# Optimization experiments

Measured on AMD Instinct MI355X. Metric: run time of the kernel, lower is better.

## Reference

```python
import math
import jax, jax.numpy as jnp
import numpy as np

B, LD, LE = 8, 512, 512
D, H, DK, F, L, V = 1024, 16, 64, 4096, 3, 32000
EPS = 1e-5
NEG = -1000000000.0


def setup_inputs() -> dict:
    key = jax.random.key(0)
    ks = jax.random.split(key, 16)
    s = 0.02
    dec_inputs = jax.random.randint(ks[0], (B, LD), 0, V)
    # causal mask: True = masked out (matches masked_fill semantics)
    self_mask = jnp.broadcast_to(jnp.triu(jnp.ones((LD, LD), bool), k=1), (B, LD, LD))
    enc_output = jax.random.normal(ks[1], (B, LE, D), jnp.float32)
    encoder_mask = jnp.zeros((B, LD, LE), bool)  # no encoder padding
    embed = jax.random.normal(ks[2], (V, D), jnp.float32) * s
    # sinusoidal positional encoding, pe[:LD]
    pos = jnp.arange(LD, dtype=jnp.float32)[:, None]
    div = jnp.exp(jnp.arange(0, D, 2, dtype=jnp.float32) * (-math.log(10000.0) / D))
    pe = jnp.zeros((LD, D), jnp.float32)
    pe = pe.at[:, 0::2].set(jnp.sin(pos * div)).at[:, 1::2].set(jnp.cos(pos * div))
    # per-layer params; axis 1 of attn params: 0=self-attn, 1=enc-dec attn
    wq = jax.random.normal(ks[3], (L, 2, D, D), jnp.float32) * s
    wk = jax.random.normal(ks[4], (L, 2, D, D), jnp.float32) * s
    wv = jax.random.normal(ks[5], (L, 2, D, D), jnp.float32) * s
    wo = jax.random.normal(ks[6], (L, 2, D, D), jnp.float32) * s
    bq = jnp.zeros((L, 2, D), jnp.float32)
    bk = jnp.zeros((L, 2, D), jnp.float32)
    bv = jnp.zeros((L, 2, D), jnp.float32)
    bo = jnp.zeros((L, 2, D), jnp.float32)
    ffn_w1 = jax.random.normal(ks[7], (L, F, D), jnp.float32) * s
    ffn_b1 = jnp.zeros((L, F), jnp.float32)
    ffn_w2 = jax.random.normal(ks[8], (L, D, F), jnp.float32) * s
    ffn_b2 = jnp.zeros((L, D), jnp.float32)
    ln_g = jnp.ones((L, 3, D), jnp.float32)   # norm1/2/3 gains
    ln_b = jnp.zeros((L, 3, D), jnp.float32)  # norm1/2/3 biases
    return dict(dec_inputs=dec_inputs, self_mask=self_mask, enc_output=enc_output,
                encoder_mask=encoder_mask, embed=embed, pe=pe,
                wq=wq, bq=bq, wk=wk, bk=bk, wv=wv, bv=bv, wo=wo, bo=bo,
                ffn_w1=ffn_w1, ffn_b1=ffn_b1, ffn_w2=ffn_w2, ffn_b2=ffn_b2,
                ln_g=ln_g, ln_b=ln_b)


def _ln(x, g, b):
    m = jnp.mean(x, axis=-1, keepdims=True)
    v = jnp.mean((x - m) ** 2, axis=-1, keepdims=True)
    return (x - m) * jax.lax.rsqrt(v + EPS) * g + b


def _mha(qi, ki, vi, mask, wq, bq, wk, bk, wv, bv, wo, bo):
    Bq, Lq, _ = qi.shape
    Lk = ki.shape[1]
    Q = (qi @ wq.T + bq).reshape(Bq, Lq, H, DK).transpose(0, 2, 1, 3)
    K = (ki @ wk.T + bk).reshape(Bq, Lk, H, DK).transpose(0, 2, 1, 3)
    Vv = (vi @ wv.T + bv).reshape(Bq, Lk, H, DK).transpose(0, 2, 1, 3)
    scores = jnp.einsum('bhqd,bhkd->bhqk', Q, K) / math.sqrt(DK)
    scores = jnp.where(mask[:, None, :, :], NEG, scores)
    attn = jax.nn.softmax(scores, axis=-1)
    ctx = jnp.einsum('bhqk,bhkd->bhqd', attn, Vv)
    ctx = ctx.transpose(0, 2, 1, 3).reshape(Bq, Lq, H * DK)
    return ctx @ wo.T + bo


def reference(dec_inputs, self_mask, enc_output, encoder_mask, embed, pe,
              wq, bq, wk, bk, wv, bv, wo, bo,
              ffn_w1, ffn_b1, ffn_w2, ffn_b2, ln_g, ln_b):
    x = embed[dec_inputs] * math.sqrt(D) + pe[None, :, :]
    for l in range(L):
        h = _ln(x, ln_g[l, 0], ln_b[l, 0])
        a = _mha(h, h, h, self_mask,
                 wq[l, 0], bq[l, 0], wk[l, 0], bk[l, 0], wv[l, 0], bv[l, 0], wo[l, 0], bo[l, 0])
        x = x + a
        h = _ln(x, ln_g[l, 1], ln_b[l, 1])
        c = _mha(h, enc_output, enc_output, encoder_mask,
                 wq[l, 1], bq[l, 1], wk[l, 1], bk[l, 1], wv[l, 1], bv[l, 1], wo[l, 1], bo[l, 1])
        x = x + c
        h = _ln(x, ln_g[l, 2], ln_b[l, 2])
        f = jax.nn.relu(h @ ffn_w1[l].T + ffn_b1[l]) @ ffn_w2[l].T + ffn_b2[l]
        # faithful quirk of the source: residual is the cross-attn output, not x
        x = c + f
    return x
```

## Files before the change

### kernel.cpp

```cpp
#include <hip/hip_runtime.h>
#include <hip/hip_bf16.h>

using bf16x8 = __attribute__((ext_vector_type(8))) short;
using f32x4  = __attribute__((ext_vector_type(4))) float;
using u16x4  = __attribute__((ext_vector_type(4))) unsigned short;

#define DEVI static __device__ __forceinline__

DEVI unsigned short f2b(float f) {
  unsigned int u = __float_as_uint(f);
  u += 0x7FFFu + ((u >> 16) & 1u);
  return (unsigned short)(u >> 16);
}

DEVI void gload16(const unsigned short* g, unsigned short* l) {
  __builtin_amdgcn_global_load_lds(
      (const __attribute__((address_space(1))) unsigned int*)g,
      (__attribute__((address_space(3))) unsigned int*)l, 16, 0, 0);
}

DEVI float wred_max16(float v) {
#pragma unroll
  for (int m = 1; m < 16; m <<= 1) v = fmaxf(v, __shfl_xor(v, m, 64));
  return v;
}
DEVI float wred_sum16(float v) {
#pragma unroll
  for (int m = 1; m < 16; m <<= 1) v += __shfl_xor(v, m, 64);
  return v;
}


__global__ void cvt_kernel(const float* __restrict__ in,
                           unsigned short* __restrict__ out, int n4) {
  int i = blockIdx.x * blockDim.x + threadIdx.x;
  const int stride = gridDim.x * blockDim.x;
  for (; i < n4; i += stride) {
    const float4 v = ((const float4*)in)[i];
    u16x4 o;
    o[0] = f2b(v.x); o[1] = f2b(v.y); o[2] = f2b(v.z); o[3] = f2b(v.w);
    ((u16x4*)out)[i] = o;
  }
}

__global__ void pack_w(const float* __restrict__ s0,
                       const float* __restrict__ s1,
                       const float* __restrict__ s2,
                       int sub, unsigned short* __restrict__ dst, int nm) {
  const int r = blockIdx.x;
  const int m = blockIdx.y;
  const int l = blockIdx.z;
  const float* src = (m == 0 ? s0 : m == 1 ? s1 : s2)
                   + (size_t)(l * 2 + sub) * 1048576 + (size_t)r * 1024;
  unsigned short* d = dst + ((size_t)(l * nm + m) * 1024 + r) * 1024;
  const int col = threadIdx.x * 4;
  const float4 v = *(const float4*)(src + col);
  u16x4 o;
  o[0] = f2b(v.x); o[1] = f2b(v.y); o[2] = f2b(v.z); o[3] = f2b(v.w);
  *(u16x4*)(d + col) = o;
}

__global__ void pack_bias(const float* __restrict__ s0,
                          const float* __restrict__ s1,
                          const float* __restrict__ s2,
                          int sub, float* __restrict__ dst, int nm) {
  const int m = blockIdx.x, l = blockIdx.y;
  const float* src = (m == 0 ? s0 : m == 1 ? s1 : s2) + (size_t)(l * 2 + sub) * 1024;
  float* d = dst + ((size_t)l * nm + m) * 1024;
  const int i = threadIdx.x * 4;
  *(float4*)(d + i) = *(const float4*)(src + i);
}

__global__ void embed_kernel(const int* __restrict__ ids,
                             const float* __restrict__ emb,
                             const float* __restrict__ pe,
                             float* __restrict__ x) {
  const int row = blockIdx.x;
  const int t = row & 511;
  const int col = threadIdx.x * 4;
  const int id = ids[row];
  const float4 e = *(const float4*)(emb + (size_t)id * 1024 + col);
  const float4 p = *(const float4*)(pe + (size_t)t * 1024 + col);
  float4 o;
  o.x = e.x * 32.f + p.x; o.y = e.y * 32.f + p.y;
  o.z = e.z * 32.f + p.z; o.w = e.w * 32.f + p.w;
  *(float4*)(x + (size_t)row * 1024 + col) = o;
}

__global__ void ln_kernel(const float* __restrict__ x,
                          const float* __restrict__ g,
                          const float* __restrict__ b,
                          unsigned short* __restrict__ out) {
  const int row = blockIdx.x;
  const int l = threadIdx.x;
  const float4* xr = (const float4*)(x + (size_t)row * 1024);
  float4 v[4];
  float s = 0.f;
#pragma unroll
  for (int i = 0; i < 4; ++i) {
    v[i] = xr[l * 4 + i];
    s += v[i].x + v[i].y + v[i].z + v[i].w;
  }
#pragma unroll
  for (int m = 1; m < 64; m <<= 1) s += __shfl_xor(s, m, 64);
  const float mean = s * (1.f / 1024.f);
  float vs = 0.f;
#pragma unroll
  for (int i = 0; i < 4; ++i) {
    float dx = v[i].x - mean, dy = v[i].y - mean, dz = v[i].z - mean, dw = v[i].w - mean;
    vs += dx * dx + dy * dy + dz * dz + dw * dw;
  }
#pragma unroll
  for (int m = 1; m < 64; m <<= 1) vs += __shfl_xor(vs, m, 64);
  const float inv = rsqrtf(vs * (1.f / 1024.f) + 1e-5f);
#pragma unroll
  for (int i = 0; i < 4; ++i) {
    const int col = l * 16 + i * 4;
    const float4 gg = *(const float4*)(g + col);
    const float4 bb = *(const float4*)(b + col);
    u16x4 o;
    o[0] = f2b((v[i].x - mean) * inv * gg.x + bb.x);
    o[1] = f2b((v[i].y - mean) * inv * gg.y + bb.y);
    o[2] = f2b((v[i].z - mean) * inv * gg.z + bb.z);
    o[3] = f2b((v[i].w - mean) * inv * gg.w + bb.w);
    *(u16x4*)(out + (size_t)row * 1024 + col) = o;
  }
}

__global__ void vt_kernel(const unsigned short* __restrict__ Vsrc, int vsd,
                          unsigned short* __restrict__ Vt) {
  __shared__ alignas(16) unsigned short t[64][72];
  const int tt = blockIdx.x;
  const int h  = blockIdx.y;
  const int b  = blockIdx.z;
  const int tid = threadIdx.x;
  const int r  = tid >> 2;
  const int ch = tid & 3;
  const unsigned short* src =
      Vsrc + (size_t)(b * 512 + tt * 64 + r) * vsd + (size_t)h * 64 + ch * 16;
  const bf16x8 v0 = *(const bf16x8*)src;
  const bf16x8 v1 = *(const bf16x8*)(src + 8);
#pragma unroll
  for (int j = 0; j < 8; ++j) {
    t[ch * 16 + j][r]     = (unsigned short)v0[j];
    t[ch * 16 + 8 + j][r] = (unsigned short)v1[j];
  }
  __syncthreads();
  const int d  = tid >> 2;
  const int tp = tid & 3;
  unsigned short* dst = Vt + (((size_t)(b * 16 + h) * 64 + d) * 512) + tt * 64 + tp * 16;
  *(bf16x8*)dst       = *(const bf16x8*)&t[d][tp * 16];
  *(bf16x8*)(dst + 8) = *(const bf16x8*)&t[d][tp * 16 + 8];
}


template<int EPI>
__global__ __launch_bounds__(512, 2) void gemm256(
    const unsigned short* __restrict__ A,
    const unsigned short* __restrict__ Bw,
    const float* __restrict__ bias,
    int N, unsigned short* __restrict__ out0) {
  constexpr int K = 1024, NK = 16;
  __shared__ alignas(16) unsigned short As0[256 * 64];
  __shared__ alignas(16) unsigned short As1[256 * 64];
  __shared__ alignas(16) unsigned short As2[256 * 64];
  __shared__ alignas(16) unsigned short Bs0[128 * 64];
  __shared__ alignas(16) unsigned short Bs1[128 * 64];
  __shared__ alignas(16) unsigned short Bs2[128 * 64];
  const int tid = threadIdx.x;
  const int lane = tid & 63;
  const int wave = tid >> 6;
  const int wr = wave >> 2;
  const int wc = wave & 3;
  int id = blockIdx.x;
  const int nwg = gridDim.x;
  id = (id & 7) * (nwg >> 3) + (id >> 3);
  const int nn = N >> 7;
  const int bx = id % nn;
  const int by = id / nn;
  const int m0 = by * 256;
  const int n0 = bx * 128;
  const int ro = lane & 15;
  const int hi = lane >> 4;

  auto stageA = [&](unsigned short* dst, int kt) {
    const size_t k0 = (size_t)kt * 64;
#pragma unroll
    for (int i = 0; i < 4; ++i) {
      const int c = tid + 512 * i;
      const int row = c >> 3;
      const int lc = (c & 7) ^ (row & 7);
      gload16(A + (size_t)(m0 + row) * K + k0 + lc * 8, dst + c * 8);
    }
  };
  auto stageB = [&](unsigned short* dst, int kt) {
    const size_t k0 = (size_t)kt * 64;
#pragma unroll
    for (int i = 0; i < 2; ++i) {
      const int c = tid + 512 * i;
      const int row = c >> 3;
      const int lc = (c & 7) ^ (row & 7);
      gload16(Bw + (size_t)(n0 + row) * K + k0 + lc * 8, dst + c * 8);
    }
  };

  f32x4 acc[8][2];
#pragma unroll
  for (int i = 0; i < 8; ++i)
#pragma unroll
    for (int j = 0; j < 2; ++j) acc[i][j] = f32x4{0.f, 0.f, 0.f, 0.f};

  stageA(As0, 0); stageB(Bs0, 0);
  stageA(As1, 1); stageB(Bs1, 1);

  auto body = [&](int kt, const unsigned short* Ac, const unsigned short* Bc,
                  unsigned short* An, unsigned short* Bn, bool last) {
    if (last) asm volatile("s_waitcnt vmcnt(0)" ::: "memory");
    else      asm volatile("s_waitcnt vmcnt(6)" ::: "memory");
    __builtin_amdgcn_s_barrier();
    if (kt + 2 < NK) { stageA(An, kt + 2); stageB(Bn, kt + 2); }
    bf16x8 af[8][2], bf[2][2];
#pragma unroll
    for (int mi = 0; mi < 8; ++mi) {
      const int r = wr * 128 + mi * 16 + ro;
#pragma unroll
      for (int ks = 0; ks < 2; ++ks)
        af[mi][ks] = *(const bf16x8*)&Ac[r * 64 + (((ks << 2) + hi) ^ (r & 7)) * 8];
    }
#pragma unroll
    for (int nj = 0; nj < 2; ++nj) {
      const int r = wc * 32 + nj * 16 + ro;
#pragma unroll
      for (int ks = 0; ks < 2; ++ks)
        bf[nj][ks] = *(const bf16x8*)&Bc[r * 64 + (((ks << 2) + hi) ^ (r & 7)) * 8];
    }
    __builtin_amdgcn_s_setprio(1);
#pragma unroll
    for (int ks = 0; ks < 2; ++ks)
#pragma unroll
      for (int mi = 0; mi < 8; ++mi)
#pragma unroll
        for (int nj = 0; nj < 2; ++nj)
          acc[mi][nj] = __builtin_amdgcn_mfma_f32_16x16x32_bf16(af[mi][ks], bf[nj][ks], acc[mi][nj], 0, 0, 0);
    __builtin_amdgcn_s_setprio(0);
  };

  for (int base = 0; base < 15; base += 3) {
    body(base,     As0, Bs0, As2, Bs2, false);
    body(base + 1, As1, Bs1, As0, Bs0, false);
    body(base + 2, As2, Bs2, As1, Bs1, false);
  }
  body(15, As0, Bs0, As1, Bs1, true);

  const int r4 = hi * 4;
#pragma unroll
  for (int mi = 0; mi < 8; ++mi) {
#pragma unroll
    for (int nj = 0; nj < 2; ++nj) {
      const int cg = n0 + wc * 32 + nj * 16 + ro;
      const float bv = bias[cg];
#pragma unroll
      for (int q = 0; q < 4; ++q) {
        const int rg = m0 + wr * 128 + mi * 16 + r4 + q;
        const float v = acc[mi][nj][q] + bv;
        out0[(size_t)rg * N + cg] = f2b(EPI == 1 ? fmaxf(v, 0.f) : v);
      }
    }
  }
}


enum { EPI_BF16 = 0, EPI_RELU_BF16 = 1, EPI_RES = 2, EPI_RES2 = 3 };

template<int EPI, int BM, int BN>
__global__ void gemm_bt(const unsigned short* __restrict__ A,
                        const unsigned short* __restrict__ Bw,
                        const float* __restrict__ bias,
                        int N, int K, int nn,
                        void* out0, const float* res, float* out1) {
  constexpr int MI = BM / 32;
  constexpr int NJ = BN / 32;
  __shared__ alignas(16) unsigned short As[2][BM * 64];
  __shared__ alignas(16) unsigned short Bs[2][BN * 64];
  const int tid = threadIdx.x;
  const int lane = tid & 63;
  const int wave = tid >> 6;
  int id = blockIdx.x;
  const int nwg = gridDim.x;
  id = (id & 7) * (nwg >> 3) + (id >> 3);
  const int bx = id % nn;
  const int by = id / nn;
  const int m0 = by * BM;
  const int n0 = bx * BN;
  const int wm = (wave >> 1) * (BM / 2);
  const int wn = (wave & 1) * (BN / 2);

  auto stage = [&](int buf, int kt) {
    const size_t k0 = (size_t)kt * 64;
#pragma unroll
    for (int i = 0; i < MI; ++i) {
      const int c = tid + 256 * i;
      const int row = c >> 3;
      const int lc = (c & 7) ^ (row & 7);
      gload16(A + (size_t)(m0 + row) * K + k0 + lc * 8, &As[buf][c * 8]);
    }
#pragma unroll
    for (int i = 0; i < NJ; ++i) {
      const int c = tid + 256 * i;
      const int row = c >> 3;
      const int lc = (c & 7) ^ (row & 7);
      gload16(Bw + (size_t)(n0 + row) * K + k0 + lc * 8, &Bs[buf][c * 8]);
    }
  };

  f32x4 acc[MI][NJ];
#pragma unroll
  for (int i = 0; i < MI; ++i)
#pragma unroll
    for (int j = 0; j < NJ; ++j) acc[i][j] = f32x4{0.f, 0.f, 0.f, 0.f};

  const int nk = K >> 6;
  stage(0, 0);
  int cur = 0;
  const int ro = lane & 15;
  const int hi = lane >> 4;
  for (int kt = 0; kt < nk; ++kt) {
    __syncthreads();
    if (kt + 1 < nk) stage(cur ^ 1, kt + 1);
    bf16x8 af[MI][2], bf[NJ][2];
#pragma unroll
    for (int i = 0; i < MI; ++i) {
      const int r = wm + i * 16 + ro;
#pragma unroll
      for (int ks = 0; ks < 2; ++ks)
        af[i][ks] = *(const bf16x8*)&As[cur][r * 64 + (((ks << 2) + hi) ^ (r & 7)) * 8];
    }
#pragma unroll
    for (int j = 0; j < NJ; ++j) {
      const int r = wn + j * 16 + ro;
#pragma unroll
      for (int ks = 0; ks < 2; ++ks)
        bf[j][ks] = *(const bf16x8*)&Bs[cur][r * 64 + (((ks << 2) + hi) ^ (r & 7)) * 8];
    }
#pragma unroll
    for (int ks = 0; ks < 2; ++ks)
#pragma unroll
      for (int i = 0; i < MI; ++i)
#pragma unroll
        for (int j = 0; j < NJ; ++j)
          acc[i][j] = __builtin_amdgcn_mfma_f32_16x16x32_bf16(af[i][ks], bf[j][ks], acc[i][j], 0, 0, 0);
    cur ^= 1;
  }

  const int r4 = hi * 4;
#pragma unroll
  for (int i = 0; i < MI; ++i) {
#pragma unroll
    for (int j = 0; j < NJ; ++j) {
      const int cg = n0 + wn + j * 16 + ro;
      const float bv = bias[cg];
#pragma unroll
      for (int q = 0; q < 4; ++q) {
        const int rg = m0 + wm + i * 16 + r4 + q;
        const size_t idx = (size_t)rg * N + cg;
        const float v = acc[i][j][q] + bv;
        if (EPI == EPI_BF16) {
          ((unsigned short*)out0)[idx] = f2b(v);
        } else if (EPI == EPI_RELU_BF16) {
          ((unsigned short*)out0)[idx] = f2b(fmaxf(v, 0.f));
        } else if (EPI == EPI_RES) {
          ((float*)out0)[idx] = res[idx] + v;
        } else {
          const float r = res[idx];
          ((float*)out0)[idx] = v;
          out1[idx] = r + v;
        }
      }
    }
  }
}


template<bool CAUSAL>
__global__ __launch_bounds__(256) void attn_kernel(
    const unsigned short* __restrict__ Qg, int qs,
    const unsigned short* __restrict__ Kg, int ksd,
    const unsigned short* __restrict__ Vt,
    unsigned short* __restrict__ Og) {
  __shared__ alignas(16) unsigned short Ks[2][64 * 64];
  __shared__ alignas(16) unsigned short Vs[2][64 * 64];
  __shared__ alignas(16) unsigned short Pl[4][32 * 64];
  const int qt0 = blockIdx.x;
  const int h  = blockIdx.y;
  const int b  = blockIdx.z;
  const int tid = threadIdx.x;
  const int lane = tid & 63;
  const int w = tid >> 6;
  const int ro = lane & 15;
  const int hi = lane >> 4;
  const int qrow0 = qt0 * 128 + w * 32;
  const size_t qbase = (size_t)b * 512 * qs  + (size_t)h * 64;
  const size_t kbase = (size_t)b * 512 * ksd + (size_t)h * 64;
  const size_t vbase = ((size_t)(b * 16 + h)) * 64 * 512;
  const size_t obase = (size_t)b * 512 * 1024 + (size_t)h * 64;

  bf16x8 qf[2][2];
#pragma unroll
  for (int mi = 0; mi < 2; ++mi)
#pragma unroll
    for (int ks = 0; ks < 2; ++ks)
      qf[mi][ks] = *(const bf16x8*)&Qg[qbase + (size_t)(qrow0 + mi * 16 + ro) * qs + ks * 32 + hi * 8];

  f32x4 o[2][4];
  float mrun[2][4], lrun[2][4];
#pragma unroll
  for (int mi = 0; mi < 2; ++mi) {
#pragma unroll
    for (int di = 0; di < 4; ++di) o[mi][di] = f32x4{0.f, 0.f, 0.f, 0.f};
#pragma unroll
    for (int q = 0; q < 4; ++q) { mrun[mi][q] = -1e30f; lrun[mi][q] = 0.f; }
  }

  auto stage = [&](int buf, int kt) {
#pragma unroll
    for (int i = 0; i < 2; ++i) {
      const int c = tid + 256 * i;
      const int row = c >> 3;
      const int lc = (c & 7) ^ (row & 7);
      gload16(Kg + kbase + (size_t)(kt * 64 + row) * ksd + lc * 8, &Ks[buf][c * 8]);
    }
#pragma unroll
    for (int i = 0; i < 2; ++i) {
      const int c = tid + 256 * i;
      const int row = c >> 3;
      const int lc = (c & 7) ^ (row & 7);
      gload16(Vt + vbase + (size_t)row * 512 + (size_t)kt * 64 + lc * 8, &Vs[buf][c * 8]);
    }
  };

  const int ktmax = CAUSAL ? (qt0 * 2 + 1) : 7;
  stage(0, 0);
  int cur = 0;
  for (int kt = 0; kt <= ktmax; ++kt) {
    __syncthreads();
    if (kt < ktmax) stage(cur ^ 1, kt + 1);
    const bool skip = CAUSAL && (kt * 64 > qrow0 + 31);
    if (!skip) {
      bf16x8 kf[4][2];
#pragma unroll
      for (int ni = 0; ni < 4; ++ni) {
        const int r = ni * 16 + ro;
#pragma unroll
        for (int ks = 0; ks < 2; ++ks)
          kf[ni][ks] = *(const bf16x8*)&Ks[cur][r * 64 + (((ks << 2) + hi) ^ (r & 7)) * 8];
      }

      f32x4 s[2][4];
#pragma unroll
      for (int mi = 0; mi < 2; ++mi)
#pragma unroll
        for (int ni = 0; ni < 4; ++ni) s[mi][ni] = f32x4{0.f, 0.f, 0.f, 0.f};
#pragma unroll
      for (int ks = 0; ks < 2; ++ks)
#pragma unroll
        for (int mi = 0; mi < 2; ++mi)
#pragma unroll
          for (int ni = 0; ni < 4; ++ni)
            s[mi][ni] = __builtin_amdgcn_mfma_f32_16x16x32_bf16(qf[mi][ks], kf[ni][ks], s[mi][ni], 0, 0, 0);

      const bool dm = CAUSAL && (kt * 64 + 63 > qrow0);
#pragma unroll
      for (int mi = 0; mi < 2; ++mi)
#pragma unroll
        for (int ni = 0; ni < 4; ++ni)
#pragma unroll
          for (int q = 0; q < 4; ++q) {
            float e = s[mi][ni][q] * 0.125f;
            if (dm && (kt * 64 + ni * 16 + ro) > (qrow0 + mi * 16 + hi * 4 + q)) e = -1e9f;
            s[mi][ni][q] = e;
          }

      float fac[2][4];
#pragma unroll
      for (int mi = 0; mi < 2; ++mi)
#pragma unroll
        for (int q = 0; q < 4; ++q) {
          float rm = s[mi][0][q];
#pragma unroll
          for (int ni = 1; ni < 4; ++ni) rm = fmaxf(rm, s[mi][ni][q]);
          rm = wred_max16(rm);
          const float mn = fmaxf(mrun[mi][q], rm);
          fac[mi][q] = __expf(mrun[mi][q] - mn);
          mrun[mi][q] = mn;
        }
#pragma unroll
      for (int mi = 0; mi < 2; ++mi)
#pragma unroll
        for (int q = 0; q < 4; ++q) {
          float rs = 0.f;
#pragma unroll
          for (int ni = 0; ni < 4; ++ni) {
            const float pv = __expf(s[mi][ni][q] - mrun[mi][q]);
            s[mi][ni][q] = pv;
            rs += pv;
          }
          rs = wred_sum16(rs);
          lrun[mi][q] = lrun[mi][q] * fac[mi][q] + rs;
        }
#pragma unroll
      for (int mi = 0; mi < 2; ++mi)
#pragma unroll
        for (int di = 0; di < 4; ++di)
#pragma unroll
          for (int q = 0; q < 4; ++q) o[mi][di][q] *= fac[mi][q];

#pragma unroll
      for (int mi = 0; mi < 2; ++mi)
#pragma unroll
        for (int ni = 0; ni < 4; ++ni)
#pragma unroll
          for (int q = 0; q < 4; ++q) {
            const int row = mi * 16 + hi * 4 + q;
            const int col = ni * 16 + ro;
            const int sc  = ((col >> 3) ^ (row & 7)) * 8 + (col & 7);
            Pl[w][row * 64 + sc] = f2b(s[mi][ni][q]);
          }

      bf16x8 pa[2][2];
#pragma unroll
      for (int mi = 0; mi < 2; ++mi)
#pragma unroll
        for (int ks = 0; ks < 2; ++ks) {
          const int row = mi * 16 + ro;
          pa[mi][ks] = *(const bf16x8*)&Pl[w][row * 64 + (((ks << 2) + hi) ^ (row & 7)) * 8];
        }

#pragma unroll
      for (int di = 0; di < 4; ++di)
#pragma unroll
        for (int ks = 0; ks < 2; ++ks) {
          const int r = di * 16 + ro;
          const bf16x8 vf = *(const bf16x8*)&Vs[cur][r * 64 + (((ks << 2) + hi) ^ (r & 7)) * 8];
#pragma unroll
          for (int mi = 0; mi < 2; ++mi)
            o[mi][di] = __builtin_amdgcn_mfma_f32_16x16x32_bf16(pa[mi][ks], vf, o[mi][di], 0, 0, 0);
        }
    }
    cur ^= 1;
  }

#pragma unroll
  for (int mi = 0; mi < 2; ++mi)
#pragma unroll
    for (int di = 0; di < 4; ++di)
#pragma unroll
      for (int q = 0; q < 4; ++q) {
        const float val = o[mi][di][q] / lrun[mi][q];
        Og[obase + (size_t)(qrow0 + mi * 16 + hi * 4 + q) * 1024 + di * 16 + ro] = f2b(val);
      }
}


extern "C" void kernel_launch(void* const* d_in, const int* in_sizes, int n_in,
                              void* d_out, int out_size, void* d_ws, size_t ws_size,
                              hipStream_t stream) {
  (void)in_sizes; (void)n_in; (void)out_size; (void)ws_size;
  const int*   dec = (const int*)d_in[0];
  const float* enc = (const float*)d_in[2];
  const float* emb = (const float*)d_in[4];
  const float* pe  = (const float*)d_in[5];
  const float* wq  = (const float*)d_in[6];
  const float* bq  = (const float*)d_in[7];
  const float* wk  = (const float*)d_in[8];
  const float* bk  = (const float*)d_in[9];
  const float* wv  = (const float*)d_in[10];
  const float* bv  = (const float*)d_in[11];
  const float* wo  = (const float*)d_in[12];
  const float* bo  = (const float*)d_in[13];
  const float* w1  = (const float*)d_in[14];
  const float* b1  = (const float*)d_in[15];
  const float* w2  = (const float*)d_in[16];
  const float* b2  = (const float*)d_in[17];
  const float* lng = (const float*)d_in[18];
  const float* lnb = (const float*)d_in[19];

  const size_t SZ_ACT = 4194304ull;

  char* p = (char*)d_ws;
  auto alloc = [&](size_t bytes) { char* r = p; p += (bytes + 255) & ~(size_t)255; return r; };
  unsigned short* qkvw  = (unsigned short*)alloc(3ull * 3 * 1048576 * 2);
  unsigned short* kvw   = (unsigned short*)alloc(3ull * 2 * 1048576 * 2);
  unsigned short* wqxb  = (unsigned short*)alloc(3ull * 1048576 * 2);
  unsigned short* Wob   = (unsigned short*)alloc(6291456ull * 2);
  unsigned short* W1b   = (unsigned short*)alloc(12582912ull * 2);
  unsigned short* W2b   = (unsigned short*)alloc(12582912ull * 2);
  unsigned short* encb  = (unsigned short*)alloc(SZ_ACT * 2);
  float*          x     = (float*)alloc(SZ_ACT * 4);
  float*          c     = (float*)alloc(SZ_ACT * 4);
  unsigned short* hb    = (unsigned short*)alloc(SZ_ACT * 2);
  unsigned short* qkvb  = (unsigned short*)alloc(4096ull * 3072 * 2);
  unsigned short* kvb   = (unsigned short*)alloc(4096ull * 6144 * 2);
  unsigned short* qb    = (unsigned short*)alloc(SZ_ACT * 2);
  unsigned short* vtb   = (unsigned short*)alloc(SZ_ACT * 2);
  unsigned short* mid   = (unsigned short*)alloc(4096ull * 4096 * 2);
  float*          qkvbias = (float*)alloc(3ull * 3072 * 4);
  float*          kvbias  = (float*)alloc(3ull * 2048 * 4);

  cvt_kernel<<<2048, 256, 0, stream>>>(wo, Wob, 1572864);
  cvt_kernel<<<2048, 256, 0, stream>>>(w1, W1b, 3145728);
  cvt_kernel<<<2048, 256, 0, stream>>>(w2, W2b, 3145728);
  cvt_kernel<<<2048, 256, 0, stream>>>(enc, encb, 1048576);
  pack_w<<<dim3(1024, 3, 3), 256, 0, stream>>>(wq, wk, wv, 0, qkvw, 3);
  pack_w<<<dim3(1024, 2, 3), 256, 0, stream>>>(wk, wv, wv, 1, kvw, 2);
  pack_w<<<dim3(1024, 1, 3), 256, 0, stream>>>(wq, wq, wq, 1, wqxb, 1);
  pack_bias<<<dim3(3, 3), 256, 0, stream>>>(bq, bk, bv, 0, qkvbias, 3);
  pack_bias<<<dim3(2, 3), 256, 0, stream>>>(bk, bv, bv, 1, kvbias, 2);
  embed_kernel<<<4096, 256, 0, stream>>>(dec, emb, pe, x);

  gemm256<0><<<48 * 16, 512, 0, stream>>>(encb, kvw, kvbias, 6144, kvb);

  const dim3 gAttn(4, 16, 8);
  const dim3 gVt(8, 16, 8);

  for (int l = 0; l < 3; ++l) {
    const float* g0 = lng + (l * 3 + 0) * 1024; const float* e0 = lnb + (l * 3 + 0) * 1024;
    const float* g1 = lng + (l * 3 + 1) * 1024; const float* e1 = lnb + (l * 3 + 1) * 1024;
    const float* g2 = lng + (l * 3 + 2) * 1024; const float* e2 = lnb + (l * 3 + 2) * 1024;

    ln_kernel<<<4096, 64, 0, stream>>>(x, g0, e0, hb);
    gemm256<0><<<24 * 16, 512, 0, stream>>>(hb, qkvw + (size_t)l * 3 * 1048576,
        qkvbias + l * 3072, 3072, qkvb);
    vt_kernel<<<gVt, 256, 0, stream>>>(qkvb + 2048, 3072, vtb);
    attn_kernel<true><<<gAttn, 256, 0, stream>>>(qkvb, 3072, qkvb + 1024, 3072, vtb, hb);
    gemm_bt<EPI_RES, 128, 64><<<32 * 16, 256, 0, stream>>>(hb, Wob + (size_t)(l * 2) * 1048576,
        bo + (l * 2) * 1024, 1024, 1024, 16, x, x, nullptr);

    ln_kernel<<<4096, 64, 0, stream>>>(x, g1, e1, hb);
    gemm_bt<EPI_BF16, 128, 64><<<32 * 16, 256, 0, stream>>>(hb, wqxb + (size_t)l * 1048576,
        bq + (l * 2 + 1) * 1024, 1024, 1024, 16, qb, nullptr, nullptr);
    vt_kernel<<<gVt, 256, 0, stream>>>(kvb + l * 2048 + 1024, 6144, vtb);
    attn_kernel<false><<<gAttn, 256, 0, stream>>>(qb, 1024, kvb + l * 2048, 6144, vtb, hb);
    gemm_bt<EPI_RES2, 128, 64><<<32 * 16, 256, 0, stream>>>(hb, Wob + (size_t)(l * 2 + 1) * 1048576,
        bo + (l * 2 + 1) * 1024, 1024, 1024, 16, c, x, x);

    ln_kernel<<<4096, 64, 0, stream>>>(x, g2, e2, hb);
    gemm256<1><<<32 * 16, 512, 0, stream>>>(hb, W1b + (size_t)l * 4194304,
        b1 + l * 4096, 4096, mid);
    float* xout = (l == 2) ? (float*)d_out : x;
    gemm_bt<EPI_RES, 128, 64><<<32 * 16, 256, 0, stream>>>(mid, W2b + (size_t)l * 4194304,
        b2 + l * 1024, 1024, 4096, 16, xout, c, nullptr);
  }
}
```

Baseline: 1.140 ms.

## Split-K the FFN down-projection GEMM with a separate reduction kernel

Replaces the FFN second GEMM (K=4096, N=1024) with a split-K=2 kernel that launches 1024 workgroups, each writing fp32 partials to a scratch buffer. A separate kernel then sums the two partials with the bias and residual. The aim is to fill more compute units, since the original 512-tile grid underuses the GPU. In exchange it adds roughly 50MB of extra fp32 partial traffic and one more kernel launch per layer.

Result: slower. 1.206 ms (+5.8%).

```diff
diff --git a/kernel.cpp b/kernel.cpp
--- a/kernel.cpp
+++ b/kernel.cpp
@@ -381,6 +381,124 @@
 }
 
 
+__global__ void gemm_sk(const unsigned short* __restrict__ A,
+                        const unsigned short* __restrict__ Bw,
+                        float* __restrict__ pbuf) {
+  constexpr int BM = 128, BN = 64, MI = 4, NJ = 2, LDA = 4096;
+  __shared__ alignas(16) unsigned short As[2][BM * 64];
+  __shared__ alignas(16) unsigned short Bs[2][BN * 64];
+  const int tid = threadIdx.x;
+  const int lane = tid & 63;
+  const int wave = tid >> 6;
+  int id = blockIdx.x;
+  const int nwg = gridDim.x;
+  id = (id & 7) * (nwg >> 3) + (id >> 3);
+  const int s  = id >> 9;
+  const int r9 = id & 511;
+  const int bx = r9 & 15;
+  const int by = r9 >> 4;
+  const int m0 = by * BM;
+  const int n0 = bx * BN;
+  const int kofs = s * 2048;
+  const int wm = (wave >> 1) * 64;
+  const int wn = (wave & 1) * 32;
+
+  auto stage = [&](int buf, int kt) {
+    const size_t k0 = (size_t)(kofs + kt * 64);
+#pragma unroll
+    for (int i = 0; i < MI; ++i) {
+      const int c = tid + 256 * i;
+      const int row = c >> 3;
+      const int lc = (c & 7) ^ (row & 7);
+      gload16(A + (size_t)(m0 + row) * LDA + k0 + lc * 8, &As[buf][c * 8]);
+    }
+#pragma unroll
+    for (int i = 0; i < NJ; ++i) {
+      const int c = tid + 256 * i;
+      const int row = c >> 3;
+      const int lc = (c & 7) ^ (row & 7);
+      gload16(Bw + (size_t)(n0 + row) * LDA + k0 + lc * 8, &Bs[buf][c * 8]);
+    }
+  };
+
+  f32x4 acc[MI][NJ];
+#pragma unroll
+  for (int i = 0; i < MI; ++i)
+#pragma unroll
+    for (int j = 0; j < NJ; ++j) acc[i][j] = f32x4{0.f, 0.f, 0.f, 0.f};
+
+  const int nk = 32;
+  stage(0, 0);
+  int cur = 0;
+  const int ro = lane & 15;
+  const int hi = lane >> 4;
+  for (int kt = 0; kt < nk; ++kt) {
+    __syncthreads();
+    if (kt + 1 < nk) stage(cur ^ 1, kt + 1);
+    bf16x8 af[MI][2], bf[NJ][2];
+#pragma unroll
+    for (int i = 0; i < MI; ++i) {
+      const int r = wm + i * 16 + ro;
+#pragma unroll
+      for (int ks = 0; ks < 2; ++ks)
+        af[i][ks] = *(const bf16x8*)&As[cur][r * 64 + (((ks << 2) + hi) ^ (r & 7)) * 8];
+    }
+#pragma unroll
+    for (int j = 0; j < NJ; ++j) {
+      const int r = wn + j * 16 + ro;
+#pragma unroll
+      for (int ks = 0; ks < 2; ++ks)
+        bf[j][ks] = *(const bf16x8*)&Bs[cur][r * 64 + (((ks << 2) + hi) ^ (r & 7)) * 8];
+    }
+#pragma unroll
+    for (int ks = 0; ks < 2; ++ks)
+#pragma unroll
+      for (int i = 0; i < MI; ++i)
+#pragma unroll
+        for (int j = 0; j < NJ; ++j)
+          acc[i][j] = __builtin_amdgcn_mfma_f32_16x16x32_bf16(af[i][ks], bf[j][ks], acc[i][j], 0, 0, 0);
+    cur ^= 1;
+  }
+
+  float* out = pbuf + (size_t)s * 4096 * 1024;
+  const int r4 = hi * 4;
+#pragma unroll
+  for (int i = 0; i < MI; ++i)
+#pragma unroll
+    for (int j = 0; j < NJ; ++j) {
+      const int cg = n0 + wn + j * 16 + ro;
+#pragma unroll
+      for (int q = 0; q < 4; ++q) {
+        const int rg = m0 + wm + i * 16 + r4 + q;
+        out[(size_t)rg * 1024 + cg] = acc[i][j][q];
+      }
+    }
+}
+
+__global__ void reduce2_kernel(const float* __restrict__ c,
+                               const float* __restrict__ pbuf,
+                               const float* __restrict__ bias,
+                               float* __restrict__ xout) {
+  const int n4 = 4096 * 1024 / 4;
+  int i = blockIdx.x * blockDim.x + threadIdx.x;
+  const int stride = gridDim.x * blockDim.x;
+  const float4* p0 = (const float4*)pbuf;
+  const float4* p1 = (const float4*)(pbuf + 4096 * 1024);
+  for (; i < n4; i += stride) {
+    const float4 cc = ((const float4*)c)[i];
+    const float4 a0 = p0[i];
+    const float4 a1 = p1[i];
+    const float4 bb = ((const float4*)bias)[i & 255];
+    float4 o;
+    o.x = cc.x + a0.x + a1.x + bb.x;
+    o.y = cc.y + a0.y + a1.y + bb.y;
+    o.z = cc.z + a0.z + a1.z + bb.z;
+    o.w = cc.w + a0.w + a1.w + bb.w;
+    ((float4*)xout)[i] = o;
+  }
+}
+
+
 template<bool CAUSAL>
 __global__ __launch_bounds__(256) void attn_kernel(
     const unsigned short* __restrict__ Qg, int qs,
@@ -603,6 +721,7 @@
   unsigned short* qb    = (unsigned short*)alloc(SZ_ACT * 2);
   unsigned short* vtb   = (unsigned short*)alloc(SZ_ACT * 2);
   unsigned short* mid   = (unsigned short*)alloc(4096ull * 4096 * 2);
+  float*          pbuf  = (float*)alloc(2ull * SZ_ACT * 4);
   float*          qkvbias = (float*)alloc(3ull * 3072 * 4);
   float*          kvbias  = (float*)alloc(3ull * 2048 * 4);
 
@@ -646,8 +765,8 @@
     ln_kernel<<<4096, 64, 0, stream>>>(x, g2, e2, hb);
     gemm256<1><<<32 * 16, 512, 0, stream>>>(hb, W1b + (size_t)l * 4194304,
         b1 + l * 4096, 4096, mid);
+    gemm_sk<<<1024, 256, 0, stream>>>(mid, W2b + (size_t)l * 4194304, pbuf);
     float* xout = (l == 2) ? (float*)d_out : x;
-    gemm_bt<EPI_RES, 128, 64><<<32 * 16, 256, 0, stream>>>(mid, W2b + (size_t)l * 4194304,
-        b2 + l * 1024, 1024, 4096, 16, xout, c, nullptr);
-  }
-}
+    reduce2_kernel<<<2048, 256, 0, stream>>>(c, pbuf, b2 + l * 1024, xout);
+  }
+}
```

## Replace 256x128 GEMM with 256x256 8-phase ping-pong pipelined kernel

Applied to the files above, without the earlier changes.

The 256x128 triple-buffered GEMM is replaced with a 256x256-tile kernel that uses two LDS buffers (even and odd). Each k-tile is split into four quarter MFMA phases, with global-to-LDS loads for later tiles issued in between phases and barriers around each phase. The larger tile roughly doubles arithmetic intensity per LDS byte and halves the number of workgroups. The cost is one block per CU (full LDS use), more barriers, and fewer workgroups: 192 for the QKV GEMM, which may underfill the 256 CUs.

New measurement: 1.112 ms. 2.4% less time.

```diff
diff --git a/kernel.cpp b/kernel.cpp
--- a/kernel.cpp
+++ b/kernel.cpp
@@ -6,6 +6,7 @@
 using u16x4  = __attribute__((ext_vector_type(4))) unsigned short;
 
 #define DEVI static __device__ __forceinline__
+#define SBAR() asm volatile("s_barrier" ::: "memory")
 
 DEVI unsigned short f2b(float f) {
   unsigned int u = __float_as_uint(f);
@@ -155,18 +156,16 @@
 
 
 template<int EPI>
-__global__ __launch_bounds__(512, 2) void gemm256(
+__global__ __launch_bounds__(512, 1) void gemm8p(
     const unsigned short* __restrict__ A,
     const unsigned short* __restrict__ Bw,
     const float* __restrict__ bias,
     int N, unsigned short* __restrict__ out0) {
-  constexpr int K = 1024, NK = 16;
-  __shared__ alignas(16) unsigned short As0[256 * 64];
-  __shared__ alignas(16) unsigned short As1[256 * 64];
-  __shared__ alignas(16) unsigned short As2[256 * 64];
-  __shared__ alignas(16) unsigned short Bs0[128 * 64];
-  __shared__ alignas(16) unsigned short Bs1[128 * 64];
-  __shared__ alignas(16) unsigned short Bs2[128 * 64];
+  constexpr int K = 1024, NT = 16;
+  __shared__ alignas(16) unsigned short AsE[256 * 64];
+  __shared__ alignas(16) unsigned short BsE[256 * 64];
+  __shared__ alignas(16) unsigned short AsO[256 * 64];
+  __shared__ alignas(16) unsigned short BsO[256 * 64];
   const int tid = threadIdx.x;
   const int lane = tid & 63;
   const int wave = tid >> 6;
@@ -175,89 +174,132 @@
   int id = blockIdx.x;
   const int nwg = gridDim.x;
   id = (id & 7) * (nwg >> 3) + (id >> 3);
-  const int nn = N >> 7;
+  const int nn = N >> 8;
   const int bx = id % nn;
   const int by = id / nn;
   const int m0 = by * 256;
-  const int n0 = bx * 128;
+  const int n0 = bx * 256;
   const int ro = lane & 15;
   const int hi = lane >> 4;
 
-  auto stageA = [&](unsigned short* dst, int kt) {
-    const size_t k0 = (size_t)kt * 64;
-#pragma unroll
-    for (int i = 0; i < 4; ++i) {
-      const int c = tid + 512 * i;
-      const int row = c >> 3;
-      const int lc = (c & 7) ^ (row & 7);
-      gload16(A + (size_t)(m0 + row) * K + k0 + lc * 8, dst + c * 8);
-    }
-  };
-  auto stageB = [&](unsigned short* dst, int kt) {
-    const size_t k0 = (size_t)kt * 64;
-#pragma unroll
-    for (int i = 0; i < 2; ++i) {
-      const int c = tid + 512 * i;
-      const int row = c >> 3;
-      const int lc = (c & 7) ^ (row & 7);
-      gload16(Bw + (size_t)(n0 + row) * K + k0 + lc * 8, dst + c * 8);
-    }
-  };
-
-  f32x4 acc[8][2];
+  auto stA = [&](unsigned short* buf, int q, int kt) {
+    const int row = tid >> 3;
+    const int lc = (tid & 7) ^ (row & 7);
+    gload16(A + (size_t)(m0 + q * 64 + row) * K + (size_t)kt * 64 + lc * 8,
+            buf + q * 4096 + tid * 8);
+  };
+  auto stB = [&](unsigned short* buf, int q, int kt) {
+    const int row = tid >> 3;
+    const int lc = (tid & 7) ^ (row & 7);
+    gload16(Bw + (size_t)(n0 + q * 64 + row) * K + (size_t)kt * 64 + lc * 8,
+            buf + q * 4096 + tid * 8);
+  };
+
+  f32x4 acc[8][4];
 #pragma unroll
   for (int i = 0; i < 8; ++i)
 #pragma unroll
-    for (int j = 0; j < 2; ++j) acc[i][j] = f32x4{0.f, 0.f, 0.f, 0.f};
-
-  stageA(As0, 0); stageB(Bs0, 0);
-  stageA(As1, 1); stageB(Bs1, 1);
-
-  auto body = [&](int kt, const unsigned short* Ac, const unsigned short* Bc,
-                  unsigned short* An, unsigned short* Bn, bool last) {
-    if (last) asm volatile("s_waitcnt vmcnt(0)" ::: "memory");
-    else      asm volatile("s_waitcnt vmcnt(6)" ::: "memory");
-    __builtin_amdgcn_s_barrier();
-    if (kt + 2 < NK) { stageA(An, kt + 2); stageB(Bn, kt + 2); }
-    bf16x8 af[8][2], bf[2][2];
-#pragma unroll
-    for (int mi = 0; mi < 8; ++mi) {
+    for (int j = 0; j < 4; ++j) acc[i][j] = f32x4{0.f, 0.f, 0.f, 0.f};
+
+  bf16x8 af[4][2], bfL[2][2], bfR[2][2];
+
+  auto ldAL = [&](const unsigned short* buf) {
+#pragma unroll
+    for (int mi = 0; mi < 4; ++mi) {
       const int r = wr * 128 + mi * 16 + ro;
 #pragma unroll
       for (int ks = 0; ks < 2; ++ks)
-        af[mi][ks] = *(const bf16x8*)&Ac[r * 64 + (((ks << 2) + hi) ^ (r & 7)) * 8];
-    }
+        af[mi][ks] = *(const bf16x8*)&buf[r * 64 + (((ks << 2) + hi) ^ (r & 7)) * 8];
+    }
+  };
+  auto ldAH = [&](const unsigned short* buf) {
+#pragma unroll
+    for (int mi = 0; mi < 4; ++mi) {
+      const int r = wr * 128 + 64 + mi * 16 + ro;
+#pragma unroll
+      for (int ks = 0; ks < 2; ++ks)
+        af[mi][ks] = *(const bf16x8*)&buf[r * 64 + (((ks << 2) + hi) ^ (r & 7)) * 8];
+    }
+  };
+  auto ldBL = [&](const unsigned short* buf) {
 #pragma unroll
     for (int nj = 0; nj < 2; ++nj) {
-      const int r = wc * 32 + nj * 16 + ro;
+      const int r = wc * 64 + nj * 16 + ro;
 #pragma unroll
       for (int ks = 0; ks < 2; ++ks)
-        bf[nj][ks] = *(const bf16x8*)&Bc[r * 64 + (((ks << 2) + hi) ^ (r & 7)) * 8];
-    }
+        bfL[nj][ks] = *(const bf16x8*)&buf[r * 64 + (((ks << 2) + hi) ^ (r & 7)) * 8];
+    }
+  };
+  auto ldBR = [&](const unsigned short* buf) {
+#pragma unroll
+    for (int nj = 0; nj < 2; ++nj) {
+      const int r = wc * 64 + 32 + nj * 16 + ro;
+#pragma unroll
+      for (int ks = 0; ks < 2; ++ks)
+        bfR[nj][ks] = *(const bf16x8*)&buf[r * 64 + (((ks << 2) + hi) ^ (r & 7)) * 8];
+    }
+  };
+  auto mmQ = [&](bf16x8 (&bf)[2][2], int mo, int no) {
     __builtin_amdgcn_s_setprio(1);
 #pragma unroll
     for (int ks = 0; ks < 2; ++ks)
 #pragma unroll
-      for (int mi = 0; mi < 8; ++mi)
+      for (int mi = 0; mi < 4; ++mi)
 #pragma unroll
         for (int nj = 0; nj < 2; ++nj)
-          acc[mi][nj] = __builtin_amdgcn_mfma_f32_16x16x32_bf16(af[mi][ks], bf[nj][ks], acc[mi][nj], 0, 0, 0);
+          acc[mo + mi][no + nj] =
+              __builtin_amdgcn_mfma_f32_16x16x32_bf16(af[mi][ks], bf[nj][ks],
+                                                      acc[mo + mi][no + nj], 0, 0, 0);
     __builtin_amdgcn_s_setprio(0);
   };
 
-  for (int base = 0; base < 15; base += 3) {
-    body(base,     As0, Bs0, As2, Bs2, false);
-    body(base + 1, As1, Bs1, As0, Bs0, false);
-    body(base + 2, As2, Bs2, As1, Bs1, false);
-  }
-  body(15, As0, Bs0, As1, Bs1, true);
+  stA(AsE, 0, 0); stA(AsE, 1, 0); stA(AsE, 2, 0); stA(AsE, 3, 0);
+  stB(BsE, 0, 0); stB(BsE, 1, 0); stB(BsE, 2, 0); stB(BsE, 3, 0);
+  stA(AsO, 0, 1); stA(AsO, 1, 1); stA(AsO, 2, 1); stA(AsO, 3, 1);
+  stB(BsO, 0, 1); stB(BsO, 1, 1);
+  asm volatile("s_waitcnt vmcnt(0)" ::: "memory");
+  SBAR();
+
+  for (int t = 0; t < NT; t += 2) {
+    const bool last = (t + 2 >= NT);
+    ldAL(AsE); ldBL(BsE);
+    stB(BsO, 2, t + 1); stB(BsO, 3, t + 1);
+    SBAR(); mmQ(bfL, 0, 0); SBAR();
+    ldBR(BsE);
+    if (!last) { stA(AsE, 0, t + 2); stA(AsE, 2, t + 2); }
+    SBAR(); mmQ(bfR, 0, 2); SBAR();
+    ldAH(AsE);
+    if (!last) { stB(BsE, 0, t + 2); stB(BsE, 1, t + 2); }
+    SBAR(); mmQ(bfL, 4, 0); SBAR();
+    if (!last) {
+      stA(AsE, 1, t + 2); stA(AsE, 3, t + 2);
+      asm volatile("s_waitcnt vmcnt(6)" ::: "memory");
+    } else {
+      asm volatile("s_waitcnt vmcnt(0)" ::: "memory");
+    }
+    SBAR(); mmQ(bfR, 4, 2); SBAR();
+    ldAL(AsO); ldBL(BsO);
+    if (!last) { stB(BsE, 2, t + 2); stB(BsE, 3, t + 2); }
+    SBAR(); mmQ(bfL, 0, 0); SBAR();
+    ldBR(BsO);
+    if (!last) { stA(AsO, 0, t + 3); stA(AsO, 2, t + 3); }
+    SBAR(); mmQ(bfR, 0, 2); SBAR();
+    ldAH(AsO);
+    if (!last) { stB(BsO, 0, t + 3); stB(BsO, 1, t + 3); }
+    SBAR(); mmQ(bfL, 4, 0); SBAR();
+    if (!last) {
+      stA(AsO, 1, t + 3); stA(AsO, 3, t + 3);
+      asm volatile("s_waitcnt vmcnt(6)" ::: "memory");
+    }
+    SBAR(); mmQ(bfR, 4, 2); SBAR();
+  }
 
   const int r4 = hi * 4;
 #pragma unroll
   for (int mi = 0; mi < 8; ++mi) {
 #pragma unroll
-    for (int nj = 0; nj < 2; ++nj) {
-      const int cg = n0 + wc * 32 + nj * 16 + ro;
+    for (int nj = 0; nj < 4; ++nj) {
+      const int cg = n0 + wc * 64 + nj * 16 + ro;
       const float bv = bias[cg];
 #pragma unroll
       for (int q = 0; q < 4; ++q) {
@@ -617,7 +659,7 @@
   pack_bias<<<dim3(2, 3), 256, 0, stream>>>(bk, bv, bv, 1, kvbias, 2);
   embed_kernel<<<4096, 256, 0, stream>>>(dec, emb, pe, x);
 
-  gemm256<0><<<48 * 16, 512, 0, stream>>>(encb, kvw, kvbias, 6144, kvb);
+  gemm8p<0><<<16 * 24, 512, 0, stream>>>(encb, kvw, kvbias, 6144, kvb);
 
   const dim3 gAttn(4, 16, 8);
   const dim3 gVt(8, 16, 8);
@@ -628,7 +670,7 @@
     const float* g2 = lng + (l * 3 + 2) * 1024; const float* e2 = lnb + (l * 3 + 2) * 1024;
 
     ln_kernel<<<4096, 64, 0, stream>>>(x, g0, e0, hb);
-    gemm256<0><<<24 * 16, 512, 0, stream>>>(hb, qkvw + (size_t)l * 3 * 1048576,
+    gemm8p<0><<<16 * 12, 512, 0, stream>>>(hb, qkvw + (size_t)l * 3 * 1048576,
         qkvbias + l * 3072, 3072, qkvb);
     vt_kernel<<<gVt, 256, 0, stream>>>(qkvb + 2048, 3072, vtb);
     attn_kernel<true><<<gAttn, 256, 0, stream>>>(qkvb, 3072, qkvb + 1024, 3072, vtb, hb);
@@ -644,7 +686,7 @@
         bo + (l * 2 + 1) * 1024, 1024, 1024, 16, c, x, x);
 
     ln_kernel<<<4096, 64, 0, stream>>>(x, g2, e2, hb);
-    gemm256<1><<<32 * 16, 512, 0, stream>>>(hb, W1b + (size_t)l * 4194304,
+    gemm8p<1><<<16 * 16, 512, 0, stream>>>(hb, W1b + (size_t)l * 4194304,
         b1 + l * 4096, 4096, mid);
     float* xout = (l == 2) ? (float*)d_out : x;
     gemm_bt<EPI_RES, 128, 64><<<32 * 16, 256, 0, stream>>>(mid, W2b + (size_t)l * 4194304,
```
